# Optimization experiments

Hardware: AMD Instinct MI355X
Metric: run time of the kernel (lower is better)

Reference implementation:

```python
import jax, jax.numpy as jnp
import numpy as np

K_HOPS = 10
ALPHA = 0.1
N_NODES = 50000
N_EDGES = 600000
F_IN = 128
HIDDEN = 64
N_CLASSES = 40


def setup_inputs() -> dict:
    key = jax.random.key(0)
    k1, k2, k3, k4 = jax.random.split(key, 4)
    x = jax.random.normal(k1, (N_NODES, F_IN), dtype=jnp.float32)
    edge_index = jax.random.randint(k2, (2, N_EDGES), 0, N_NODES, dtype=jnp.int32)
    edge_weight = jnp.ones((N_EDGES,), dtype=jnp.float32)
    W1 = jax.random.normal(k3, (F_IN, HIDDEN), dtype=jnp.float32) * (1.0 / np.sqrt(F_IN))
    b1 = jnp.zeros((HIDDEN,), dtype=jnp.float32)
    W2 = jax.random.normal(k4, (HIDDEN, N_CLASSES), dtype=jnp.float32) * (1.0 / np.sqrt(HIDDEN))
    b2 = jnp.zeros((N_CLASSES,), dtype=jnp.float32)
    return {"x": x, "edge_index": edge_index, "edge_weight": edge_weight,
            "W1": W1, "b1": b1, "W2": W2, "b2": b2}


def reference(x, edge_index, edge_weight, W1, b1, W2, b2):
    n = x.shape[0]
    # GCN symmetric normalization with self-loops (tfg gcn cache)
    self_idx = jnp.arange(n, dtype=edge_index.dtype)
    row = jnp.concatenate([edge_index[0], self_idx])
    col = jnp.concatenate([edge_index[1], self_idx])
    w = jnp.concatenate([edge_weight, jnp.ones((n,), dtype=edge_weight.dtype)])
    deg = jax.ops.segment_sum(w, row, num_segments=n)
    dinv = jnp.where(deg > 0, jax.lax.rsqrt(jnp.maximum(deg, 1e-12)), 0.0)
    nw = dinv[row] * w * dinv[col]  # [E+N] normalized edge weights

    def prop(h):
        # h_out[i] = sum_{(i,j)} nw * h[j]
        return jax.ops.segment_sum(h[col] * nw[:, None], row, num_segments=n)

    def step(h, _):
        h_next = prop(h)
        return h_next, None

    # SSGC: out = (1-alpha)/K * sum_{l=1..K} T^l x + alpha * x
    def step_acc(carry, _):
        h, acc = carry
        h_next = prop(h)
        return (h_next, acc + h_next), None

    (_, acc), _ = jax.lax.scan(step_acc, (x, jnp.zeros_like(x)), None, length=K_HOPS)
    h = (1.0 - ALPHA) / K_HOPS * acc + ALPHA * x  # [N, F]

    h = jax.nn.relu(h @ W1 + b1)  # [N, HIDDEN]
    logits = h @ W2 + b2          # [N, N_CLASSES]
    return logits
```

## Files before the change

### kernel.cpp

```cpp
#include <hip/hip_runtime.h>
#include <hip/hip_fp16.h>
#include <math.h>

constexpr int   N   = 50000;
constexpr int   E   = 600000;
constexpr int   FIN = 128;
constexpr int   H   = 64;
constexpr int   C   = 40;
constexpr int   K   = 10;
constexpr float CK  = (1.0f - 0.1f) / 10.0f;
constexpr float AL  = 0.1f;

typedef float v2f __attribute__((ext_vector_type(2)));

__device__ __forceinline__ unsigned pack_fp8x4(float f0, float f1, float f2, float f3) {
    unsigned r = __builtin_amdgcn_cvt_pk_fp8_f32(f0, f1, 0u, false);
    r = __builtin_amdgcn_cvt_pk_fp8_f32(f2, f3, r, true);
    return r;
}

__device__ __forceinline__ float ep_w(unsigned v) {
    return __half2float(__ushort_as_half((unsigned short)(v >> 16)));
}
__device__ __forceinline__ unsigned ep_pack(int c, float w) {
    return (unsigned)(unsigned short)c |
           ((unsigned)__half_as_ushort(__float2half_rn(w)) << 16);
}

__device__ __forceinline__ void accum8(float* s, uint2 v, float w) {
    v2f p0 = __builtin_amdgcn_cvt_pk_f32_fp8(v.x, false);
    v2f p1 = __builtin_amdgcn_cvt_pk_f32_fp8(v.x, true);
    v2f p2 = __builtin_amdgcn_cvt_pk_f32_fp8(v.y, false);
    v2f p3 = __builtin_amdgcn_cvt_pk_f32_fp8(v.y, true);
    s[0] = fmaf(w, p0.x, s[0]); s[1] = fmaf(w, p0.y, s[1]);
    s[2] = fmaf(w, p1.x, s[2]); s[3] = fmaf(w, p1.y, s[3]);
    s[4] = fmaf(w, p2.x, s[4]); s[5] = fmaf(w, p2.y, s[5]);
    s[6] = fmaf(w, p3.x, s[6]); s[7] = fmaf(w, p3.y, s[7]);
}

constexpr int G1N  = 64;
constexpr int XPAD = 132;
__global__ __launch_bounds__(256, 2) void k_gemm1(const float* __restrict__ x,
                                                  const float* __restrict__ W1,
                                                  float* __restrict__ y0,
                                                  unsigned char* __restrict__ y0f8) {
    __shared__ float ws[FIN * H];
    __shared__ float xs[G1N * XPAD];
    const float4* W14 = (const float4*)W1;
    const float4* x4  = (const float4*)x;
    int t = threadIdx.x;
    int node0 = blockIdx.x * G1N;
    for (int i = t; i < FIN * H / 4; i += 256) ((float4*)ws)[i] = W14[i];
    for (int p = 0; p < 8; ++p) {
        int idx = p * 256 + t;
        int n   = idx >> 5;
        int kk  = idx & 31;
        int node = node0 + n;
        float4 v = (node < N) ? x4[(size_t)node * (FIN / 4) + kk]
                              : make_float4(0.f, 0.f, 0.f, 0.f);
        *(float4*)(xs + n * XPAD + kk * 4) = v;
    }
    __syncthreads();
    int nb = (t >> 4) * 4;
    int cb = (t & 15) * 4;
    float a00=0,a01=0,a02=0,a03=0, a10=0,a11=0,a12=0,a13=0;
    float a20=0,a21=0,a22=0,a23=0, a30=0,a31=0,a32=0,a33=0;
#pragma unroll 8
    for (int k = 0; k < FIN; ++k) {
        float4 wv = *(const float4*)(ws + k * H + cb);
        float x0 = xs[(nb + 0) * XPAD + k];
        float x1 = xs[(nb + 1) * XPAD + k];
        float x2 = xs[(nb + 2) * XPAD + k];
        float x3 = xs[(nb + 3) * XPAD + k];
        a00 = fmaf(x0, wv.x, a00); a01 = fmaf(x0, wv.y, a01);
        a02 = fmaf(x0, wv.z, a02); a03 = fmaf(x0, wv.w, a03);
        a10 = fmaf(x1, wv.x, a10); a11 = fmaf(x1, wv.y, a11);
        a12 = fmaf(x1, wv.z, a12); a13 = fmaf(x1, wv.w, a13);
        a20 = fmaf(x2, wv.x, a20); a21 = fmaf(x2, wv.y, a21);
        a22 = fmaf(x2, wv.z, a22); a23 = fmaf(x2, wv.w, a23);
        a30 = fmaf(x3, wv.x, a30); a31 = fmaf(x3, wv.y, a31);
        a32 = fmaf(x3, wv.z, a32); a33 = fmaf(x3, wv.w, a33);
    }
    float4 rows[4] = {make_float4(a00,a01,a02,a03), make_float4(a10,a11,a12,a13),
                      make_float4(a20,a21,a22,a23), make_float4(a30,a31,a32,a33)};
#pragma unroll
    for (int i = 0; i < 4; ++i) {
        int node = node0 + nb + i;
        if (node >= N) break;
        float4 r = rows[i];
        *(float4*)(y0 + (size_t)node * H + cb) = r;
        *(unsigned*)(y0f8 + (size_t)node * H + cb) = pack_fp8x4(r.x, r.y, r.z, r.w);
    }
}

__global__ void k_count(const int* __restrict__ row, int* __restrict__ cnt8) {
    int e = blockIdx.x * blockDim.x + threadIdx.x;
    if (e >= E) return;
    atomicAdd(&cnt8[(size_t)(blockIdx.x & 7) * N + row[e]], 1);
}

__global__ __launch_bounds__(1024) void k_scan_blocks(const int* __restrict__ cnt8,
                                                      int* __restrict__ row_ptr,
                                                      int* __restrict__ bsum) {
    __shared__ int s[1024];
    int gid = blockIdx.x * 1024 + threadIdx.x;
    int v = 0;
    if (gid < N) {
#pragma unroll
        for (int c = 0; c < 8; ++c) v += cnt8[(size_t)c * N + gid];
        v = (v + 3) & ~3;
    }
    s[threadIdx.x] = v;
    __syncthreads();
    for (int off = 1; off < 1024; off <<= 1) {
        int t = (threadIdx.x >= off) ? s[threadIdx.x - off] : 0;
        __syncthreads();
        s[threadIdx.x] += t;
        __syncthreads();
    }
    if (gid < N) row_ptr[gid] = s[threadIdx.x] - v;
    if (threadIdx.x == 1023) bsum[blockIdx.x] = s[1023];
}

__global__ void k_scan_sums(const int* __restrict__ bsum, int* __restrict__ boff, int nb,
                            int* __restrict__ rowN) {
    int lane = threadIdx.x;
    int orig = (lane < nb) ? bsum[lane] : 0;
    int v = orig;
    for (int off = 1; off < 64; off <<= 1) {
        int t = __shfl_up(v, off, 64);
        if (lane >= off) v += t;
    }
    if (lane < nb) boff[lane] = v - orig;
    if (lane == nb - 1) *rowN = v;
}

__global__ __launch_bounds__(1024) void k_addoff(int* __restrict__ row_ptr,
                                                 const int* __restrict__ boff,
                                                 int* __restrict__ cnt8) {
    int gid = blockIdx.x * 1024 + threadIdx.x;
    if (gid < N) {
        int rp = row_ptr[gid] + boff[blockIdx.x];
        row_ptr[gid] = rp;
        int off = rp;
#pragma unroll
        for (int c = 0; c < 8; ++c) {
            int t = cnt8[(size_t)c * N + gid];
            cnt8[(size_t)c * N + gid] = off;
            off += t;
        }
    }
}

__global__ void k_scatter(const int* __restrict__ row, const int* __restrict__ col,
                          const float* __restrict__ w,
                          int* __restrict__ off8, unsigned* __restrict__ ep) {
    int e = blockIdx.x * blockDim.x + threadIdx.x;
    if (e >= E) return;
    int r = row[e];
    int p = atomicAdd(&off8[(size_t)(blockIdx.x & 7) * N + r], 1);
    ep[p] = ep_pack(col[e], w[e]);
}

__global__ void k_deg_dinv(const unsigned* __restrict__ ep, const int* __restrict__ row_ptr,
                           float* __restrict__ dinv, float* __restrict__ dinv2) {
    int i = blockIdx.x * blockDim.x + threadIdx.x;
    if (i >= N) return;
    float d = 1.0f;
    int e0 = row_ptr[i], e1 = row_ptr[i + 1];
    for (int j = e0; j < e1; ++j) d += ep_w(ep[j]);
    float di = rsqrtf(d);
    dinv[i]  = di;
    dinv2[i] = di * di;
}

__global__ __launch_bounds__(256) void k_norm(unsigned* __restrict__ ep,
                                              const int* __restrict__ row_ptr,
                                              const float* __restrict__ dinv) {
    int node = blockIdx.x * 32 + (threadIdx.x >> 3);
    if (node >= N) return;
    int l = threadIdx.x & 7;
    float dr = dinv[node];
    int e0 = row_ptr[node], e1 = row_ptr[node + 1];
    for (int j = e0 + l; j < e1; j += 8) {
        unsigned v = ep[j];
        int c = v & 0xFFFFu;
        ep[j] = ep_pack(c, ep_w(v) * dr * dinv[c]);
    }
}

constexpr int HSP = 68;
template <bool WRITE_H, bool ACC_INIT, bool FINAL>
__global__ __launch_bounds__(256) void k_prop(const uint2* __restrict__ hin,
                                              uint2* __restrict__ hout,
                                              __half* __restrict__ acch,
                                              const float* __restrict__ dinv2,
                                              const int* __restrict__ row_ptr,
                                              const unsigned* __restrict__ ep,
                                              const float4* __restrict__ y04,
                                              const float* __restrict__ b1,
                                              const float* __restrict__ W2,
                                              const float* __restrict__ b2,
                                              float* __restrict__ out) {
    extern __shared__ float smem[];
    float* w2s = smem;
    float* hs  = smem + H * C;
    float* b2s = hs + 32 * HSP;
    float* b1s = b2s + C;
    int t = threadIdx.x;
    if (FINAL) {
        for (int i = t; i < H * C; i += 256) w2s[i] = W2[i];
        if (t < C) b2s[t] = b2[t];
        if (t < H) b1s[t] = b1[t];
        __syncthreads();
    }
    int lane = t & 63;
    int nib  = (t >> 6) * 8 + (lane >> 3);
    int l    = lane & 7;
    int node = blockIdx.x * 32 + nib;
    bool nv  = node < N;
    int nodec = nv ? node : N - 1;
    int start = row_ptr[nodec];
    int pdeg  = nv ? (row_ptr[nodec + 1] - start) : 0;
    int md = pdeg;
#pragma unroll
    for (int off = 8; off <= 32; off <<= 1) md = max(md, __shfl_xor(md, off, 64));

    uint4* ap = (uint4*)(acch + (size_t)nodec * H + l * 8);
    uint4 old;
    if (nv && (FINAL || !ACC_INIT)) old = *ap;

    float s[8];
#pragma unroll
    for (int i = 0; i < 8; ++i) s[i] = 0.f;

    const unsigned* rp = ep + start;
    uint4 e4 = *(const uint4*)rp;
    for (int batch = 0; batch < md; batch += 4) {
        uint4 cur = e4;
        int nb4  = batch + 4;
        int off4 = (nb4 < pdeg) ? nb4 : 0;
        e4 = *(const uint4*)(rp + off4);
        bool a0 = batch     < pdeg, a1 = batch + 1 < pdeg;
        bool a2 = batch + 2 < pdeg, a3 = batch + 3 < pdeg;
        uint2 v0 = hin[(size_t)(cur.x & 0xFFFFu) * 8 + l];
        uint2 v1 = hin[(size_t)(cur.y & 0xFFFFu) * 8 + l];
        uint2 v2 = hin[(size_t)(cur.z & 0xFFFFu) * 8 + l];
        uint2 v3 = hin[(size_t)(cur.w & 0xFFFFu) * 8 + l];
        accum8(s, v0, a0 ? ep_w(cur.x) : 0.0f);
        accum8(s, v1, a1 ? ep_w(cur.y) : 0.0f);
        accum8(s, v2, a2 ? ep_w(cur.z) : 0.0f);
        accum8(s, v3, a3 ? ep_w(cur.w) : 0.0f);
    }
    if (nv) {
        size_t base = (size_t)nodec * 8 + l;
        accum8(s, hin[base], dinv2[nodec]);
        if (WRITE_H) {
            uint2 o;
            o.x = pack_fp8x4(s[0], s[1], s[2], s[3]);
            o.y = pack_fp8x4(s[4], s[5], s[6], s[7]);
            hout[base] = o;
        }
        if (FINAL) {
            const unsigned* u = (const unsigned*)&old;
#pragma unroll
            for (int d = 0; d < 4; ++d) {
                float2 f = __half22float2(*(__half2*)&u[d]);
                s[2*d+0] += f.x; s[2*d+1] += f.y;
            }
            float4 ya = y04[(size_t)nodec * (H / 4) + 2 * l];
            float4 yb = y04[(size_t)nodec * (H / 4) + 2 * l + 1];
            const float* bp = b1s + l * 8;
            float* hp = hs + nib * HSP + l * 8;
            hp[0] = fmaxf(fmaf(CK, s[0], fmaf(AL, ya.x, bp[0])), 0.f);
            hp[1] = fmaxf(fmaf(CK, s[1], fmaf(AL, ya.y, bp[1])), 0.f);
            hp[2] = fmaxf(fmaf(CK, s[2], fmaf(AL, ya.z, bp[2])), 0.f);
            hp[3] = fmaxf(fmaf(CK, s[3], fmaf(AL, ya.w, bp[3])), 0.f);
            hp[4] = fmaxf(fmaf(CK, s[4], fmaf(AL, yb.x, bp[4])), 0.f);
            hp[5] = fmaxf(fmaf(CK, s[5], fmaf(AL, yb.y, bp[5])), 0.f);
            hp[6] = fmaxf(fmaf(CK, s[6], fmaf(AL, yb.z, bp[6])), 0.f);
            hp[7] = fmaxf(fmaf(CK, s[7], fmaf(AL, yb.w, bp[7])), 0.f);
        } else {
            if (!ACC_INIT) {
                const unsigned* u = (const unsigned*)&old;
#pragma unroll
                for (int d = 0; d < 4; ++d) {
                    float2 f = __half22float2(*(__half2*)&u[d]);
                    s[2*d+0] += f.x; s[2*d+1] += f.y;
                }
            }
            uint4 nvp;
            unsigned* u = (unsigned*)&nvp;
#pragma unroll
            for (int d = 0; d < 4; ++d) {
                __half2 h = __floats2half2_rn(s[2*d+0], s[2*d+1]);
                u[d] = *(unsigned*)&h;
            }
            *ap = nvp;
        }
    }
    if (FINAL) {
        __syncthreads();
        int node0 = blockIdx.x * 32;
        for (int o = t; o < 32 * C; o += 256) {
            int nl = o / C, c = o % C;
            int n2 = node0 + nl;
            if (n2 >= N) continue;
            float v = b2s[c];
            const float* hr = &hs[nl * HSP];
#pragma unroll
            for (int k = 0; k < H; ++k) v = fmaf(hr[k], w2s[k * C + c], v);
            out[n2 * C + c] = v;
        }
    }
}

extern "C" void kernel_launch(void* const* d_in, const int* in_sizes, int n_in,
                              void* d_out, int out_size, void* d_ws, size_t ws_size,
                              hipStream_t stream) {
    const float* x  = (const float*)d_in[0];
    const int*   ei = (const int*)d_in[1];
    const float* ew = (const float*)d_in[2];
    const float* W1 = (const float*)d_in[3];
    const float* b1 = (const float*)d_in[4];
    const float* W2 = (const float*)d_in[5];
    const float* b2 = (const float*)d_in[6];
    float* out = (float*)d_out;

    const int* row = ei;
    const int* col = ei + E;

    char* ws = (char*)d_ws;
    size_t off = 0;
    auto alloc = [&](size_t bytes) -> char* {
        char* p = ws + off;
        off = (off + bytes + 1023) & ~(size_t)1023;
        return p;
    };
    constexpr size_t EPAD = (size_t)E + 3 * (size_t)N + 1024;
    float*         y0   = (float*)alloc((size_t)N * H * 4);
    unsigned char* y0f8 = (unsigned char*)alloc((size_t)N * H);
    unsigned char* ha   = (unsigned char*)alloc((size_t)N * H);
    unsigned char* hb   = (unsigned char*)alloc((size_t)N * H);
    __half*        acch = (__half*)alloc((size_t)N * H * 2);
    int*      cnt8   = (int*)     alloc((size_t)8 * N * 4);
    float*    dinv   = (float*)   alloc((size_t)N * 4);
    float*    dinv2  = (float*)   alloc((size_t)N * 4);
    int*      row_ptr= (int*)     alloc((size_t)(N + 1) * 4);
    int*      bsum   = (int*)     alloc(64 * 4);
    int*      boff   = (int*)     alloc(64 * 4);
    unsigned* ep     = (unsigned*)alloc(EPAD * 4);

    hipMemsetAsync(cnt8, 0, (size_t)8 * N * 4, stream);
    hipMemsetAsync(ep, 0, EPAD * 4, stream);

    k_gemm1<<<(N + G1N - 1) / G1N, 256, 0, stream>>>(x, W1, y0, y0f8);

    k_count<<<(E + 255) / 256, 256, 0, stream>>>(row, cnt8);

    constexpr int NB = (N + 1023) / 1024;
    k_scan_blocks<<<NB, 1024, 0, stream>>>(cnt8, row_ptr, bsum);
    k_scan_sums<<<1, 64, 0, stream>>>(bsum, boff, NB, row_ptr + N);
    k_addoff<<<NB, 1024, 0, stream>>>(row_ptr, boff, cnt8);

    k_scatter<<<(E + 255) / 256, 256, 0, stream>>>(row, col, ew, cnt8, ep);
    k_deg_dinv<<<(N + 255) / 256, 256, 0, stream>>>(ep, row_ptr, dinv, dinv2);
    k_norm<<<(N + 31) / 32, 256, 0, stream>>>(ep, row_ptr, dinv);

    const uint2* hin = (const uint2*)y0f8;
    uint2* bufs[2] = {(uint2*)ha, (uint2*)hb};
    const float4* y04 = (const float4*)y0;
    int grid = (N + 31) / 32;
    size_t smemF = (size_t)(H * C + 32 * HSP + C + H) * 4;
    for (int hop = 0; hop < K; ++hop) {
        uint2* hout = bufs[hop & 1];
        if (hop == 0)
            k_prop<true, true, false><<<grid, 256, 0, stream>>>(hin, hout, acch, dinv2,
                row_ptr, ep, y04, b1, W2, b2, out);
        else if (hop == K - 1)
            k_prop<false, false, true><<<grid, 256, smemF, stream>>>(hin, hout, acch, dinv2,
                row_ptr, ep, y04, b1, W2, b2, out);
        else
            k_prop<true, false, false><<<grid, 256, 0, stream>>>(hin, hout, acch, dinv2,
                row_ptr, ep, y04, b1, W2, b2, out);
        hin = hout;
    }
}
```

Before: 322.7 us.

## Use 16 lanes per node in propagation and rank-based deterministic CSR scatter

The propagation kernel now gives each node 16 lanes of 4 fp8 features instead of 8 lanes of 8, processes 16 nodes per block, and prefetches two edge quads per iteration to raise memory-level parallelism on the gathers. The CSR build records each edge's rank from the counting atomic, so scatter needs no second atomic pass. The full memset of the edge array is replaced by zeroing only the per-row padding slots and the tail. The trade-off is twice as many propagation blocks, a larger edge-index load per lane, and a 16-bit rank array that limits per-copy row degree to 65535.

```diff
diff --git a/kernel.cpp b/kernel.cpp
--- a/kernel.cpp
+++ b/kernel.cpp
@@ -27,15 +27,11 @@
            ((unsigned)__half_as_ushort(__float2half_rn(w)) << 16);
 }
 
-__device__ __forceinline__ void accum8(float* s, uint2 v, float w) {
-    v2f p0 = __builtin_amdgcn_cvt_pk_f32_fp8(v.x, false);
-    v2f p1 = __builtin_amdgcn_cvt_pk_f32_fp8(v.x, true);
-    v2f p2 = __builtin_amdgcn_cvt_pk_f32_fp8(v.y, false);
-    v2f p3 = __builtin_amdgcn_cvt_pk_f32_fp8(v.y, true);
+__device__ __forceinline__ void accum4(float* s, unsigned v, float w) {
+    v2f p0 = __builtin_amdgcn_cvt_pk_f32_fp8(v, false);
+    v2f p1 = __builtin_amdgcn_cvt_pk_f32_fp8(v, true);
     s[0] = fmaf(w, p0.x, s[0]); s[1] = fmaf(w, p0.y, s[1]);
     s[2] = fmaf(w, p1.x, s[2]); s[3] = fmaf(w, p1.y, s[3]);
-    s[4] = fmaf(w, p2.x, s[4]); s[5] = fmaf(w, p2.y, s[5]);
-    s[6] = fmaf(w, p3.x, s[6]); s[7] = fmaf(w, p3.y, s[7]);
 }
 
 constexpr int G1N  = 64;
@@ -93,10 +89,20 @@
     }
 }
 
-__global__ void k_count(const int* __restrict__ row, int* __restrict__ cnt8) {
-    int e = blockIdx.x * blockDim.x + threadIdx.x;
-    if (e >= E) return;
-    atomicAdd(&cnt8[(size_t)(blockIdx.x & 7) * N + row[e]], 1);
+__global__ __launch_bounds__(256) void k_count(const int* __restrict__ row,
+                                               int* __restrict__ cnt8,
+                                               unsigned short* __restrict__ rank) {
+    int base = blockIdx.x * 1024 + threadIdx.x;
+    int copy = blockIdx.x & 7;
+#pragma unroll
+    for (int i = 0; i < 4; ++i) {
+        int e = base + i * 256;
+        if (e < E) {
+            int r = row[e];
+            int old = atomicAdd(&cnt8[(size_t)copy * N + r], 1);
+            rank[e] = (unsigned short)old;
+        }
+    }
 }
 
 __global__ __launch_bounds__(1024) void k_scan_blocks(const int* __restrict__ cnt8,
@@ -137,29 +143,47 @@
 
 __global__ __launch_bounds__(1024) void k_addoff(int* __restrict__ row_ptr,
                                                  const int* __restrict__ boff,
-                                                 int* __restrict__ cnt8) {
+                                                 int* __restrict__ cnt8,
+                                                 unsigned* __restrict__ ep) {
     int gid = blockIdx.x * 1024 + threadIdx.x;
     if (gid < N) {
         int rp = row_ptr[gid] + boff[blockIdx.x];
         row_ptr[gid] = rp;
         int off = rp;
+        int real = 0;
 #pragma unroll
         for (int c = 0; c < 8; ++c) {
             int t = cnt8[(size_t)c * N + gid];
             cnt8[(size_t)c * N + gid] = off;
             off += t;
-        }
-    }
-}
-
-__global__ void k_scatter(const int* __restrict__ row, const int* __restrict__ col,
-                          const float* __restrict__ w,
-                          int* __restrict__ off8, unsigned* __restrict__ ep) {
-    int e = blockIdx.x * blockDim.x + threadIdx.x;
-    if (e >= E) return;
-    int r = row[e];
-    int p = atomicAdd(&off8[(size_t)(blockIdx.x & 7) * N + r], 1);
-    ep[p] = ep_pack(col[e], w[e]);
+            real += t;
+        }
+        int pd = (real + 3) & ~3;
+        for (int j = real; j < pd; ++j) ep[rp + j] = 0u;
+    }
+    if (gid == 0) {
+        int tot = row_ptr[N];
+        *(uint4*)(ep + tot) = make_uint4(0u, 0u, 0u, 0u);
+    }
+}
+
+__global__ __launch_bounds__(256) void k_scatter(const int* __restrict__ row,
+                                                 const int* __restrict__ col,
+                                                 const float* __restrict__ w,
+                                                 const unsigned short* __restrict__ rank,
+                                                 const int* __restrict__ base8,
+                                                 unsigned* __restrict__ ep) {
+    int base = blockIdx.x * 1024 + threadIdx.x;
+    int copy = blockIdx.x & 7;
+#pragma unroll
+    for (int i = 0; i < 4; ++i) {
+        int e = base + i * 256;
+        if (e < E) {
+            int r = row[e];
+            int p = base8[(size_t)copy * N + r] + rank[e];
+            ep[p] = ep_pack(col[e], w[e]);
+        }
+    }
 }
 
 __global__ void k_deg_dinv(const unsigned* __restrict__ ep, const int* __restrict__ row_ptr,
@@ -191,8 +215,8 @@
 
 constexpr int HSP = 68;
 template <bool WRITE_H, bool ACC_INIT, bool FINAL>
-__global__ __launch_bounds__(256) void k_prop(const uint2* __restrict__ hin,
-                                              uint2* __restrict__ hout,
+__global__ __launch_bounds__(256) void k_prop(const unsigned* __restrict__ hin,
+                                              unsigned* __restrict__ hout,
                                               __half* __restrict__ acch,
                                               const float* __restrict__ dinv2,
                                               const int* __restrict__ row_ptr,
@@ -205,7 +229,7 @@
     extern __shared__ float smem[];
     float* w2s = smem;
     float* hs  = smem + H * C;
-    float* b2s = hs + 32 * HSP;
+    float* b2s = hs + 16 * HSP;
     float* b1s = b2s + C;
     int t = threadIdx.x;
     if (FINAL) {
@@ -215,84 +239,85 @@
         __syncthreads();
     }
     int lane = t & 63;
-    int nib  = (t >> 6) * 8 + (lane >> 3);
-    int l    = lane & 7;
-    int node = blockIdx.x * 32 + nib;
+    int nib  = (t >> 6) * 4 + (lane >> 4);
+    int l    = lane & 15;
+    int node = blockIdx.x * 16 + nib;
     bool nv  = node < N;
     int nodec = nv ? node : N - 1;
     int start = row_ptr[nodec];
     int pdeg  = nv ? (row_ptr[nodec + 1] - start) : 0;
     int md = pdeg;
 #pragma unroll
-    for (int off = 8; off <= 32; off <<= 1) md = max(md, __shfl_xor(md, off, 64));
-
-    uint4* ap = (uint4*)(acch + (size_t)nodec * H + l * 8);
-    uint4 old;
+    for (int off = 16; off <= 32; off <<= 1) md = max(md, __shfl_xor(md, off, 64));
+
+    size_t base = (size_t)nodec * 16 + l;
+    unsigned vself = hin[base];
+    float d2       = dinv2[nodec];
+    uint2* ap = (uint2*)(acch + (size_t)nodec * H + l * 4);
+    uint2 old;
     if (nv && (FINAL || !ACC_INIT)) old = *ap;
 
-    float s[8];
-#pragma unroll
-    for (int i = 0; i < 8; ++i) s[i] = 0.f;
+    float s[4];
+#pragma unroll
+    for (int i = 0; i < 4; ++i) s[i] = 0.f;
 
     const unsigned* rp = ep + start;
-    uint4 e4 = *(const uint4*)rp;
-    for (int batch = 0; batch < md; batch += 4) {
-        uint4 cur = e4;
-        int nb4  = batch + 4;
-        int off4 = (nb4 < pdeg) ? nb4 : 0;
-        e4 = *(const uint4*)(rp + off4);
-        bool a0 = batch     < pdeg, a1 = batch + 1 < pdeg;
-        bool a2 = batch + 2 < pdeg, a3 = batch + 3 < pdeg;
-        uint2 v0 = hin[(size_t)(cur.x & 0xFFFFu) * 8 + l];
-        uint2 v1 = hin[(size_t)(cur.y & 0xFFFFu) * 8 + l];
-        uint2 v2 = hin[(size_t)(cur.z & 0xFFFFu) * 8 + l];
-        uint2 v3 = hin[(size_t)(cur.w & 0xFFFFu) * 8 + l];
-        accum8(s, v0, a0 ? ep_w(cur.x) : 0.0f);
-        accum8(s, v1, a1 ? ep_w(cur.y) : 0.0f);
-        accum8(s, v2, a2 ? ep_w(cur.z) : 0.0f);
-        accum8(s, v3, a3 ? ep_w(cur.w) : 0.0f);
+    uint4 ea = *(const uint4*)rp;
+    uint4 eb = *(const uint4*)(rp + ((4 < pdeg) ? 4 : 0));
+    for (int batch = 0; batch < md; batch += 8) {
+        uint4 ca = ea, cb = eb;
+        int n0 = batch + 8, n1 = batch + 12;
+        ea = *(const uint4*)(rp + ((n0 < pdeg) ? n0 : 0));
+        eb = *(const uint4*)(rp + ((n1 < pdeg) ? n1 : 0));
+        unsigned v0 = hin[(size_t)(ca.x & 0xFFFFu) * 16 + l];
+        unsigned v1 = hin[(size_t)(ca.y & 0xFFFFu) * 16 + l];
+        unsigned v2 = hin[(size_t)(ca.z & 0xFFFFu) * 16 + l];
+        unsigned v3 = hin[(size_t)(ca.w & 0xFFFFu) * 16 + l];
+        unsigned v4 = hin[(size_t)(cb.x & 0xFFFFu) * 16 + l];
+        unsigned v5 = hin[(size_t)(cb.y & 0xFFFFu) * 16 + l];
+        unsigned v6 = hin[(size_t)(cb.z & 0xFFFFu) * 16 + l];
+        unsigned v7 = hin[(size_t)(cb.w & 0xFFFFu) * 16 + l];
+        accum4(s, v0, (batch     < pdeg) ? ep_w(ca.x) : 0.0f);
+        accum4(s, v1, (batch + 1 < pdeg) ? ep_w(ca.y) : 0.0f);
+        accum4(s, v2, (batch + 2 < pdeg) ? ep_w(ca.z) : 0.0f);
+        accum4(s, v3, (batch + 3 < pdeg) ? ep_w(ca.w) : 0.0f);
+        accum4(s, v4, (batch + 4 < pdeg) ? ep_w(cb.x) : 0.0f);
+        accum4(s, v5, (batch + 5 < pdeg) ? ep_w(cb.y) : 0.0f);
+        accum4(s, v6, (batch + 6 < pdeg) ? ep_w(cb.z) : 0.0f);
+        accum4(s, v7, (batch + 7 < pdeg) ? ep_w(cb.w) : 0.0f);
     }
     if (nv) {
-        size_t base = (size_t)nodec * 8 + l;
-        accum8(s, hin[base], dinv2[nodec]);
+        accum4(s, vself, d2);
         if (WRITE_H) {
-            uint2 o;
-            o.x = pack_fp8x4(s[0], s[1], s[2], s[3]);
-            o.y = pack_fp8x4(s[4], s[5], s[6], s[7]);
-            hout[base] = o;
+            hout[base] = pack_fp8x4(s[0], s[1], s[2], s[3]);
         }
         if (FINAL) {
             const unsigned* u = (const unsigned*)&old;
 #pragma unroll
-            for (int d = 0; d < 4; ++d) {
+            for (int d = 0; d < 2; ++d) {
                 float2 f = __half22float2(*(__half2*)&u[d]);
                 s[2*d+0] += f.x; s[2*d+1] += f.y;
             }
-            float4 ya = y04[(size_t)nodec * (H / 4) + 2 * l];
-            float4 yb = y04[(size_t)nodec * (H / 4) + 2 * l + 1];
-            const float* bp = b1s + l * 8;
-            float* hp = hs + nib * HSP + l * 8;
+            float4 ya = y04[(size_t)nodec * (H / 4) + l];
+            const float* bp = b1s + l * 4;
+            float* hp = hs + nib * HSP + l * 4;
             hp[0] = fmaxf(fmaf(CK, s[0], fmaf(AL, ya.x, bp[0])), 0.f);
             hp[1] = fmaxf(fmaf(CK, s[1], fmaf(AL, ya.y, bp[1])), 0.f);
             hp[2] = fmaxf(fmaf(CK, s[2], fmaf(AL, ya.z, bp[2])), 0.f);
             hp[3] = fmaxf(fmaf(CK, s[3], fmaf(AL, ya.w, bp[3])), 0.f);
-            hp[4] = fmaxf(fmaf(CK, s[4], fmaf(AL, yb.x, bp[4])), 0.f);
-            hp[5] = fmaxf(fmaf(CK, s[5], fmaf(AL, yb.y, bp[5])), 0.f);
-            hp[6] = fmaxf(fmaf(CK, s[6], fmaf(AL, yb.z, bp[6])), 0.f);
-            hp[7] = fmaxf(fmaf(CK, s[7], fmaf(AL, yb.w, bp[7])), 0.f);
         } else {
             if (!ACC_INIT) {
                 const unsigned* u = (const unsigned*)&old;
 #pragma unroll
-                for (int d = 0; d < 4; ++d) {
+                for (int d = 0; d < 2; ++d) {
                     float2 f = __half22float2(*(__half2*)&u[d]);
                     s[2*d+0] += f.x; s[2*d+1] += f.y;
                 }
             }
-            uint4 nvp;
+            uint2 nvp;
             unsigned* u = (unsigned*)&nvp;
 #pragma unroll
-            for (int d = 0; d < 4; ++d) {
+            for (int d = 0; d < 2; ++d) {
                 __half2 h = __floats2half2_rn(s[2*d+0], s[2*d+1]);
                 u[d] = *(unsigned*)&h;
             }
@@ -301,8 +326,8 @@
     }
     if (FINAL) {
         __syncthreads();
-        int node0 = blockIdx.x * 32;
-        for (int o = t; o < 32 * C; o += 256) {
+        int node0 = blockIdx.x * 16;
+        for (int o = t; o < 16 * C; o += 256) {
             int nl = o / C, c = o % C;
             int n2 = node0 + nl;
             if (n2 >= N) continue;
@@ -338,12 +363,13 @@
         return p;
     };
     constexpr size_t EPAD = (size_t)E + 3 * (size_t)N + 1024;
-    float*         y0   = (float*)alloc((size_t)N * H * 4);
-    unsigned char* y0f8 = (unsigned char*)alloc((size_t)N * H);
-    unsigned char* ha   = (unsigned char*)alloc((size_t)N * H);
-    unsigned char* hb   = (unsigned char*)alloc((size_t)N * H);
-    __half*        acch = (__half*)alloc((size_t)N * H * 2);
-    int*      cnt8   = (int*)     alloc((size_t)8 * N * 4);
+    float*          y0   = (float*)alloc((size_t)N * H * 4);
+    unsigned char*  y0f8 = (unsigned char*)alloc((size_t)N * H);
+    unsigned char*  ha   = (unsigned char*)alloc((size_t)N * H);
+    unsigned char*  hb   = (unsigned char*)alloc((size_t)N * H);
+    __half*         acch = (__half*)alloc((size_t)N * H * 2);
+    int*            cnt8 = (int*)alloc((size_t)8 * N * 4);
+    unsigned short* rank = (unsigned short*)alloc((size_t)E * 2);
     float*    dinv   = (float*)   alloc((size_t)N * 4);
     float*    dinv2  = (float*)   alloc((size_t)N * 4);
     int*      row_ptr= (int*)     alloc((size_t)(N + 1) * 4);
@@ -352,28 +378,27 @@
     unsigned* ep     = (unsigned*)alloc(EPAD * 4);
 
     hipMemsetAsync(cnt8, 0, (size_t)8 * N * 4, stream);
-    hipMemsetAsync(ep, 0, EPAD * 4, stream);
 
     k_gemm1<<<(N + G1N - 1) / G1N, 256, 0, stream>>>(x, W1, y0, y0f8);
 
-    k_count<<<(E + 255) / 256, 256, 0, stream>>>(row, cnt8);
+    k_count<<<(E + 1023) / 1024, 256, 0, stream>>>(row, cnt8, rank);
 
     constexpr int NB = (N + 1023) / 1024;
     k_scan_blocks<<<NB, 1024, 0, stream>>>(cnt8, row_ptr, bsum);
     k_scan_sums<<<1, 64, 0, stream>>>(bsum, boff, NB, row_ptr + N);
-    k_addoff<<<NB, 1024, 0, stream>>>(row_ptr, boff, cnt8);
-
-    k_scatter<<<(E + 255) / 256, 256, 0, stream>>>(row, col, ew, cnt8, ep);
+    k_addoff<<<NB, 1024, 0, stream>>>(row_ptr, boff, cnt8, ep);
+
+    k_scatter<<<(E + 1023) / 1024, 256, 0, stream>>>(row, col, ew, rank, cnt8, ep);
     k_deg_dinv<<<(N + 255) / 256, 256, 0, stream>>>(ep, row_ptr, dinv, dinv2);
     k_norm<<<(N + 31) / 32, 256, 0, stream>>>(ep, row_ptr, dinv);
 
-    const uint2* hin = (const uint2*)y0f8;
-    uint2* bufs[2] = {(uint2*)ha, (uint2*)hb};
+    const unsigned* hin = (const unsigned*)y0f8;
+    unsigned* bufs[2] = {(unsigned*)ha, (unsigned*)hb};
     const float4* y04 = (const float4*)y0;
-    int grid = (N + 31) / 32;
-    size_t smemF = (size_t)(H * C + 32 * HSP + C + H) * 4;
+    int grid = (N + 15) / 16;
+    size_t smemF = (size_t)(H * C + 16 * HSP + C + H) * 4;
     for (int hop = 0; hop < K; ++hop) {
-        uint2* hout = bufs[hop & 1];
+        unsigned* hout = bufs[hop & 1];
         if (hop == 0)
             k_prop<true, true, false><<<grid, 256, 0, stream>>>(hin, hout, acch, dinv2,
                 row_ptr, ep, y04, b1, W2, b2, out);
```

After: 293.1 us. 9.2% less time.
